# Performance work log

Hardware: AMD Instinct MI355X
Metric: run time of the kernel (lower is better)

Reference implementation:

```python
import jax, jax.numpy as jnp
import numpy as np

IN_FEATURES = 128
OUT_FEATURES = 128
CAPACITY = 200000


def setup_inputs() -> dict:
    key = jax.random.key(0)
    k1, k2, k3 = jax.random.split(key, 3)
    query = jax.random.normal(k1, (IN_FEATURES,), dtype=jnp.float32)
    keys = jax.random.normal(k2, (CAPACITY, IN_FEATURES), dtype=jnp.float32)
    values = jax.random.normal(k3, (CAPACITY, OUT_FEATURES), dtype=jnp.float32)
    return {"query": query, "keys": keys, "values": values}


def reference(query, keys, values):
    # Negative L1 distance from query to each stored key: [N]
    diffs = -jnp.sum(jnp.abs(keys - query[None, :]), axis=1)
    # Softmax attention over all stored entries
    attention = jax.nn.softmax(diffs, axis=0)
    # Weighted sum of values: [out_features]
    out = attention @ values
    return out
```

## Files before the change

kernel.cpp:

```cpp
#include <hip/hip_runtime.h>
#include <math.h>

#define DIM 128
#define PSTRIDE 132
#define NEG_BIG (-3.0e38f)
#define THRESH 20.0f

__global__ __launch_bounds__(256, 2) void nd_logits(const float* __restrict__ query,
                                                    const float* __restrict__ keys,
                                                    float* __restrict__ logits,
                                                    float* __restrict__ wsmax,
                                                    int nrows, int nchunks, int P) {
    const int tid  = threadIdx.x;
    const int lane = tid & 63;
    const int quad = lane & 3;
    const int rsub = lane >> 2;
    const int wid  = blockIdx.x * (blockDim.x >> 6) + (tid >> 6);

    float4 qv[8];
    #pragma unroll
    for (int j = 0; j < 8; ++j)
        qv[j] = *reinterpret_cast<const float4*>(query + quad * 4 + j * 16);

    const int q  = nchunks / P, r = nchunks % P;
    const int c0 = wid * q + (wid < r ? wid : r);
    const int c1 = c0 + q + (wid < r ? 1 : 0);

    float wmax = NEG_BIG;

    #define LBODY(cc)                                                             \
        {                                                                         \
            const int  row = (cc) * 16 + rsub;                                    \
            const bool ok  = row < nrows;                                         \
            const int  rr  = ok ? row : (nrows - 1);                              \
            const float* kp = keys + (size_t)rr * DIM + quad * 4;                 \
            float4 kv[8];                                                         \
            _Pragma("unroll")                                                     \
            for (int j = 0; j < 8; ++j)                                           \
                kv[j] = *reinterpret_cast<const float4*>(kp + j * 16);            \
            float s = 0.f;                                                        \
            _Pragma("unroll")                                                     \
            for (int j = 0; j < 8; ++j)                                           \
                s += fabsf(kv[j].x - qv[j].x) + fabsf(kv[j].y - qv[j].y)          \
                   + fabsf(kv[j].z - qv[j].z) + fabsf(kv[j].w - qv[j].w);         \
            s += __shfl_xor(s, 1, 64);                                            \
            s += __shfl_xor(s, 2, 64);                                            \
            const float lg = ok ? -s : NEG_BIG;                                   \
            wmax = fmaxf(wmax, lg);                                               \
            if (quad == 0 && ok) logits[row] = lg;                                \
        }

    int c = c0;
    for (; c + 1 < c1; c += 2) { LBODY(c) LBODY(c + 1) }
    if (c < c1) LBODY(c)
    #undef LBODY

    #pragma unroll
    for (int off = 4; off < 64; off <<= 1)
        wmax = fmaxf(wmax, __shfl_xor(wmax, off, 64));
    if (lane == 0) wsmax[wid] = wmax;
}

__global__ __launch_bounds__(256) void nd_accum(const float* __restrict__ values,
                                                const float* __restrict__ logits,
                                                const float* __restrict__ wsmax,
                                                float* __restrict__ part,
                                                int nrows, int P, int NW) {
    __shared__ float sh4[4];
    __shared__ float shM;
    const int tid  = threadIdx.x;
    const int lane = tid & 63;
    const int wid  = blockIdx.x * (blockDim.x >> 6) + (tid >> 6);

    float m = NEG_BIG;
    for (int i = tid; i < P; i += 256) m = fmaxf(m, wsmax[i]);
    #pragma unroll
    for (int off = 1; off < 64; off <<= 1)
        m = fmaxf(m, __shfl_xor(m, off, 64));
    if ((tid & 63) == 0) sh4[tid >> 6] = m;
    __syncthreads();
    if (tid == 0) shM = fmaxf(fmaxf(sh4[0], sh4[1]), fmaxf(sh4[2], sh4[3]));
    __syncthreads();
    const float M   = shM;
    const float cut = M - THRESH;

    float  l = 0.f;
    float2 acc = make_float2(0.f, 0.f);

    for (int base = wid * 64; base < nrows; base += NW * 64) {
        const int  row   = base + lane;
        const bool valid = row < nrows;
        const float lg   = valid ? logits[row] : NEG_BIG;
        const float w    = __expf(lg - M);
        l += w;
        unsigned long long ball = __ballot(valid && lg >= cut);
        while (ball) {
            const int b1 = __builtin_ctzll(ball); ball &= ball - 1;
            int b2 = -1;
            if (ball) { b2 = __builtin_ctzll(ball); ball &= ball - 1; }
            const float  w1 = __shfl(w, b1, 64);
            const float2 v1 = *reinterpret_cast<const float2*>(
                                  values + (size_t)(base + b1) * DIM + lane * 2);
            float  w2 = 0.f;
            float2 v2 = make_float2(0.f, 0.f);
            if (b2 >= 0) {
                w2 = __shfl(w, b2, 64);
                v2 = *reinterpret_cast<const float2*>(
                         values + (size_t)(base + b2) * DIM + lane * 2);
            }
            acc.x += w1 * v1.x + w2 * v2.x;
            acc.y += w1 * v1.y + w2 * v2.y;
        }
    }

    #pragma unroll
    for (int off = 1; off < 64; off <<= 1)
        l += __shfl_xor(l, off, 64);

    float* wp = part + (size_t)wid * PSTRIDE;
    if (lane == 0) wp[0] = l;
    *reinterpret_cast<float2*>(wp + 4 + lane * 2) = acc;
}

__global__ __launch_bounds__(256) void nd_merge(const float* __restrict__ part,
                                                float* __restrict__ part2) {
    __shared__ float sh_red[256];
    __shared__ float shL;
    const int tid  = threadIdx.x;
    const int base = blockIdx.x * 64;

    if (tid < 64) {
        float lp = part[(size_t)(base + tid) * PSTRIDE];
        #pragma unroll
        for (int off = 32; off > 0; off >>= 1)
            lp += __shfl_xor(lp, off, 64);
        if (tid == 0) shL = lp;
    }

    const int d = tid & 127, g = tid >> 7;
    float o = 0.f;
    for (int p = g; p < 64; p += 2)
        o += part[(size_t)(base + p) * PSTRIDE + 4 + d];
    sh_red[tid] = o;
    __syncthreads();

    if (tid < 128) {
        float* wp = part2 + (size_t)blockIdx.x * PSTRIDE;
        if (tid == 0) wp[0] = shL;
        wp[4 + tid] = sh_red[tid] + sh_red[tid + 128];
    }
}

__global__ __launch_bounds__(256) void nd_final(const float* __restrict__ part2,
                                                float* __restrict__ out, int B2) {
    __shared__ float sh_red[256];
    __shared__ float shL;
    const int tid = threadIdx.x;

    if (tid < 64) {
        float lp = 0.f;
        for (int p = tid; p < B2; p += 64)
            lp += part2[(size_t)p * PSTRIDE];
        #pragma unroll
        for (int off = 32; off > 0; off >>= 1)
            lp += __shfl_xor(lp, off, 64);
        if (tid == 0) shL = lp;
    }

    const int d = tid & 127, g = tid >> 7;
    float o = 0.f;
    for (int p = g; p < B2; p += 2)
        o += part2[(size_t)p * PSTRIDE + 4 + d];
    sh_red[tid] = o;
    __syncthreads();

    if (tid < 128)
        out[tid] = (sh_red[tid] + sh_red[tid + 128]) / shL;
}

extern "C" void kernel_launch(void* const* d_in, const int* in_sizes, int n_in,
                              void* d_out, int out_size, void* d_ws, size_t ws_size,
                              hipStream_t stream) {
    const float* query  = (const float*)d_in[0];
    const float* keys   = (const float*)d_in[1];
    const float* values = (const float*)d_in[2];
    float* out = (float*)d_out;
    float* ws  = (float*)d_ws;

    const int nrows   = in_sizes[1] / DIM;
    const int nchunks = (nrows + 15) / 16;
    const int LN      = (nrows + 63) & ~63;

    int P = (((nchunks + 1) / 2) + 3) & ~3;
    if (P < 256) P = 256;

    int NW = 4096;
    const size_t capf = ws_size / sizeof(float);
    while ((size_t)LN + (size_t)P + 16
           + (size_t)(NW + NW / 64) * PSTRIDE > capf && NW > 512)
        NW >>= 1;
    const int B2 = NW / 64;

    float* logits = ws;
    float* wsmax  = ws + LN;
    float* part   = wsmax + ((P + 15) & ~15);
    float* part2  = part + (size_t)NW * PSTRIDE;

    nd_logits<<<P / 4,  256, 0, stream>>>(query, keys, logits, wsmax, nrows, nchunks, P);
    nd_accum <<<NW / 4, 256, 0, stream>>>(values, logits, wsmax, part, nrows, P, NW);
    nd_merge <<<B2,     256, 0, stream>>>(part, part2);
    nd_final <<<1,      256, 0, stream>>>(part2, out, B2);
}
```

Before: 48.80 us.

## Assign one key row per lane in logits kernel with grid-stride tiles

Rewrites the distance kernel so each lane computes a full 128-wide L1 distance for its own row, reading the query from shared memory. This removes the intra-quad shuffles and the per-row chunk partitioning, using a fixed grid of 2048 waves that stride over 64-row tiles. The cost is that each wave's global loads now stride across 64 separate rows per instruction, which weakens coalescing and leans on cache reuse across the unrolled loads.

```diff
diff --git a/kernel.cpp b/kernel.cpp
--- a/kernel.cpp
+++ b/kernel.cpp
@@ -10,53 +10,52 @@
                                                     const float* __restrict__ keys,
                                                     float* __restrict__ logits,
                                                     float* __restrict__ wsmax,
-                                                    int nrows, int nchunks, int P) {
+                                                    int nrows, int ntiles, int P) {
+    __shared__ float qs[DIM];
     const int tid  = threadIdx.x;
     const int lane = tid & 63;
-    const int quad = lane & 3;
-    const int rsub = lane >> 2;
     const int wid  = blockIdx.x * (blockDim.x >> 6) + (tid >> 6);
 
-    float4 qv[8];
+    if (tid < 32)
+        reinterpret_cast<float4*>(qs)[tid] = reinterpret_cast<const float4*>(query)[tid];
+    __syncthreads();
+
+    float wmax = NEG_BIG;
+
+    for (int tile = wid; tile < ntiles; tile += P) {
+        const int  row = tile * 64 + lane;
+        const bool ok  = row < nrows;
+        const float* kp = keys + (size_t)(ok ? row : 0) * DIM;
+
+        float s0 = 0.f, s1 = 0.f, s2 = 0.f, s3 = 0.f;
+        #pragma unroll
+        for (int j = 0; j < 32; j += 4) {
+            const float4 k0 = *reinterpret_cast<const float4*>(kp + 4 * (j + 0));
+            const float4 k1 = *reinterpret_cast<const float4*>(kp + 4 * (j + 1));
+            const float4 k2 = *reinterpret_cast<const float4*>(kp + 4 * (j + 2));
+            const float4 k3 = *reinterpret_cast<const float4*>(kp + 4 * (j + 3));
+            const float4 q0 = *reinterpret_cast<const float4*>(qs + 4 * (j + 0));
+            const float4 q1 = *reinterpret_cast<const float4*>(qs + 4 * (j + 1));
+            const float4 q2 = *reinterpret_cast<const float4*>(qs + 4 * (j + 2));
+            const float4 q3 = *reinterpret_cast<const float4*>(qs + 4 * (j + 3));
+            s0 += fabsf(k0.x - q0.x) + fabsf(k0.y - q0.y)
+                + fabsf(k0.z - q0.z) + fabsf(k0.w - q0.w);
+            s1 += fabsf(k1.x - q1.x) + fabsf(k1.y - q1.y)
+                + fabsf(k1.z - q1.z) + fabsf(k1.w - q1.w);
+            s2 += fabsf(k2.x - q2.x) + fabsf(k2.y - q2.y)
+                + fabsf(k2.z - q2.z) + fabsf(k2.w - q2.w);
+            s3 += fabsf(k3.x - q3.x) + fabsf(k3.y - q3.y)
+                + fabsf(k3.z - q3.z) + fabsf(k3.w - q3.w);
+        }
+        const float lg = -((s0 + s1) + (s2 + s3));
+        if (ok) {
+            logits[row] = lg;
+            wmax = fmaxf(wmax, lg);
+        }
+    }
+
     #pragma unroll
-    for (int j = 0; j < 8; ++j)
-        qv[j] = *reinterpret_cast<const float4*>(query + quad * 4 + j * 16);
-
-    const int q  = nchunks / P, r = nchunks % P;
-    const int c0 = wid * q + (wid < r ? wid : r);
-    const int c1 = c0 + q + (wid < r ? 1 : 0);
-
-    float wmax = NEG_BIG;
-
-    #define LBODY(cc)                                                             \
-        {                                                                         \
-            const int  row = (cc) * 16 + rsub;                                    \
-            const bool ok  = row < nrows;                                         \
-            const int  rr  = ok ? row : (nrows - 1);                              \
-            const float* kp = keys + (size_t)rr * DIM + quad * 4;                 \
-            float4 kv[8];                                                         \
-            _Pragma("unroll")                                                     \
-            for (int j = 0; j < 8; ++j)                                           \
-                kv[j] = *reinterpret_cast<const float4*>(kp + j * 16);            \
-            float s = 0.f;                                                        \
-            _Pragma("unroll")                                                     \
-            for (int j = 0; j < 8; ++j)                                           \
-                s += fabsf(kv[j].x - qv[j].x) + fabsf(kv[j].y - qv[j].y)          \
-                   + fabsf(kv[j].z - qv[j].z) + fabsf(kv[j].w - qv[j].w);         \
-            s += __shfl_xor(s, 1, 64);                                            \
-            s += __shfl_xor(s, 2, 64);                                            \
-            const float lg = ok ? -s : NEG_BIG;                                   \
-            wmax = fmaxf(wmax, lg);                                               \
-            if (quad == 0 && ok) logits[row] = lg;                                \
-        }
-
-    int c = c0;
-    for (; c + 1 < c1; c += 2) { LBODY(c) LBODY(c + 1) }
-    if (c < c1) LBODY(c)
-    #undef LBODY
-
-    #pragma unroll
-    for (int off = 4; off < 64; off <<= 1)
+    for (int off = 1; off < 64; off <<= 1)
         wmax = fmaxf(wmax, __shfl_xor(wmax, off, 64));
     if (lane == 0) wsmax[wid] = wmax;
 }
@@ -187,12 +186,11 @@
     float* out = (float*)d_out;
     float* ws  = (float*)d_ws;
 
-    const int nrows   = in_sizes[1] / DIM;
-    const int nchunks = (nrows + 15) / 16;
-    const int LN      = (nrows + 63) & ~63;
-
-    int P = (((nchunks + 1) / 2) + 3) & ~3;
-    if (P < 256) P = 256;
+    const int nrows  = in_sizes[1] / DIM;
+    const int ntiles = (nrows + 63) / 64;
+    const int LN     = (nrows + 63) & ~63;
+
+    const int P = 2048;
 
     int NW = 4096;
     const size_t capf = ws_size / sizeof(float);
@@ -206,7 +204,7 @@
     float* part   = wsmax + ((P + 15) & ~15);
     float* part2  = part + (size_t)NW * PSTRIDE;
 
-    nd_logits<<<P / 4,  256, 0, stream>>>(query, keys, logits, wsmax, nrows, nchunks, P);
+    nd_logits<<<P / 4,  256, 0, stream>>>(query, keys, logits, wsmax, nrows, ntiles, P);
     nd_accum <<<NW / 4, 256, 0, stream>>>(values, logits, wsmax, part, nrows, P, NW);
     nd_merge <<<B2,     256, 0, stream>>>(part, part2);
     nd_final <<<1,      256, 0, stream>>>(part2, out, B2);
```

Measured after the change: 66.90 us. +37.1%, slower.
